# Optimization experiments

Hardware: AMD Instinct MI355X
Metric: run time of the kernel (lower is better)

Reference implementation:

```python
import jax, jax.numpy as jnp
import numpy as np

N, DIM, EMB = 8192, 128, 16
WIDTHS = [64, 32, 16]


def setup_inputs() -> dict:
    key = jax.random.key(0)
    ks = jax.random.split(key, 16)
    x = jax.random.normal(ks[0], (N, DIM), dtype=jnp.float32)
    dims = [DIM] + WIDTHS + [EMB]  # 128 -> 64 -> 32 -> 16 -> 16
    params = {}
    for i in range(4):
        fan_in, fan_out = dims[i], dims[i + 1]
        params[f"W{i+1}"] = jax.random.normal(ks[1 + 2 * i], (fan_in, fan_out), dtype=jnp.float32) * (1.0 / np.sqrt(fan_in))
        params[f"b{i+1}"] = jax.random.normal(ks[2 + 2 * i], (fan_out,), dtype=jnp.float32) * 0.01
    return {"x": x, **params}


def _encode(x, W1, b1, W2, b2, W3, b3, W4, b4):
    h = jax.nn.relu(x @ W1 + b1)
    h = jax.nn.relu(h @ W2 + b2)
    h = jax.nn.relu(h @ W3 + b3)
    return h @ W4 + b4  # [N, EMB]


def _tstudent_probs(z):
    # squared euclidean distances via the norm trick (avoids [N,N,EMB] tensor)
    sq = jnp.sum(z * z, axis=1)  # [N]
    dist = jnp.maximum(sq[:, None] + sq[None, :] - 2.0 * (z @ z.T), 0.0)  # [N,N]
    numerator = 1.0 / (1.0 + dist)
    return numerator / jnp.sum(numerator, axis=1, keepdims=True)


def reference(x, W1, b1, W2, b2, W3, b3, W4, b4):
    z = _encode(x, W1, b1, W2, b2, W3, b3, W4, b4)
    return _tstudent_probs(z)
```

## Files before the change

kernel.cpp:

```cpp
#include <hip/hip_runtime.h>

#define N 8192
#define DIM 128
#define NCHUNK 32

__global__ __launch_bounds__(64) void encoder_kernel(
    const float* __restrict__ x,
    const float* __restrict__ W1, const float* __restrict__ b1,
    const float* __restrict__ W2, const float* __restrict__ b2,
    const float* __restrict__ W3, const float* __restrict__ b3,
    const float* __restrict__ W4, const float* __restrict__ b4,
    float* __restrict__ z, float* __restrict__ sqout)
{
    __shared__ float sW2[64 * 32];
    __shared__ float sW3[32 * 16];
    __shared__ float sW4[16 * 16];
    __shared__ float sb1[64];
    __shared__ float sb2[32];
    __shared__ float sb3[16];
    __shared__ float sb4[16];
    __shared__ float sW1[128 * 64];
    __shared__ float sh1[64 * 65];

    int t = threadIdx.x;
    float* sh2 = sW1;
    float* sh3 = sW1 + 2112;

    for (int idx = t; idx < 128 * 64; idx += 64) sW1[idx] = W1[idx];
    for (int idx = t; idx < 64 * 32; idx += 64) sW2[idx] = W2[idx];
    for (int idx = t; idx < 32 * 16; idx += 64) sW3[idx] = W3[idx];
    for (int idx = t; idx < 16 * 16; idx += 64) sW4[idx] = W4[idx];
    sb1[t] = b1[t];
    if (t < 32) sb2[t] = b2[t];
    if (t < 16) { sb3[t] = b3[t]; sb4[t] = b4[t]; }
    __syncthreads();

    int row = blockIdx.x * 64 + t;
    const float4* xr = (const float4*)(x + (size_t)row * DIM);

    float h1[64];
    #pragma unroll
    for (int k = 0; k < 64; ++k) h1[k] = sb1[k];
    for (int j4 = 0; j4 < 32; ++j4) {
        float4 xv = xr[j4];
        const float* w0 = &sW1[(j4 * 4 + 0) * 64];
        const float* w1 = &sW1[(j4 * 4 + 1) * 64];
        const float* w2 = &sW1[(j4 * 4 + 2) * 64];
        const float* w3 = &sW1[(j4 * 4 + 3) * 64];
        #pragma unroll
        for (int k = 0; k < 64; ++k) h1[k] = fmaf(xv.x, w0[k], h1[k]);
        #pragma unroll
        for (int k = 0; k < 64; ++k) h1[k] = fmaf(xv.y, w1[k], h1[k]);
        #pragma unroll
        for (int k = 0; k < 64; ++k) h1[k] = fmaf(xv.z, w2[k], h1[k]);
        #pragma unroll
        for (int k = 0; k < 64; ++k) h1[k] = fmaf(xv.w, w3[k], h1[k]);
    }
    #pragma unroll
    for (int k = 0; k < 64; ++k) sh1[t * 65 + k] = fmaxf(h1[k], 0.0f);

    float h2[32];
    #pragma unroll
    for (int k = 0; k < 32; ++k) h2[k] = sb2[k];
    for (int j = 0; j < 64; ++j) {
        float a = sh1[t * 65 + j];
        #pragma unroll
        for (int k = 0; k < 32; ++k) h2[k] = fmaf(a, sW2[j * 32 + k], h2[k]);
    }
    #pragma unroll
    for (int k = 0; k < 32; ++k) sh2[t * 33 + k] = fmaxf(h2[k], 0.0f);

    float h3[16];
    #pragma unroll
    for (int k = 0; k < 16; ++k) h3[k] = sb3[k];
    for (int j = 0; j < 32; ++j) {
        float a = sh2[t * 33 + j];
        #pragma unroll
        for (int k = 0; k < 16; ++k) h3[k] = fmaf(a, sW3[j * 16 + k], h3[k]);
    }
    #pragma unroll
    for (int k = 0; k < 16; ++k) sh3[t * 17 + k] = fmaxf(h3[k], 0.0f);

    float zo[16];
    #pragma unroll
    for (int k = 0; k < 16; ++k) zo[k] = sb4[k];
    for (int j = 0; j < 16; ++j) {
        float a = sh3[t * 17 + j];
        #pragma unroll
        for (int k = 0; k < 16; ++k) zo[k] = fmaf(a, sW4[j * 16 + k], zo[k]);
    }

    float s = 0.0f;
    #pragma unroll
    for (int k = 0; k < 16; ++k) s = fmaf(zo[k], zo[k], s);
    sqout[row] = s;
    float4* zr = (float4*)(z + (size_t)row * 16);
    zr[0] = make_float4(zo[0], zo[1], zo[2], zo[3]);
    zr[1] = make_float4(zo[4], zo[5], zo[6], zo[7]);
    zr[2] = make_float4(zo[8], zo[9], zo[10], zo[11]);
    zr[3] = make_float4(zo[12], zo[13], zo[14], zo[15]);
}

__global__ __launch_bounds__(256) void pass1_kernel(
    const float* __restrict__ z, const float* __restrict__ sq,
    float* __restrict__ partial)
{
    __shared__ float s_zj[256 * 16];
    __shared__ float s_sqj[256];

    int t = threadIdx.x;
    int i0 = blockIdx.x * 256 + t;
    int i1 = i0 + 4096;
    int jb = blockIdx.y * 256;

    {
        const float4* src = (const float4*)(z + (size_t)(jb + t) * 16);
        float4* dst = (float4*)(s_zj + t * 16);
        dst[0] = src[0]; dst[1] = src[1]; dst[2] = src[2]; dst[3] = src[3];
        s_sqj[t] = sq[jb + t];
    }

    float zi0[16], zi1[16];
    {
        const float4* p0 = (const float4*)(z + (size_t)i0 * 16);
        const float4* p1 = (const float4*)(z + (size_t)i1 * 16);
        #pragma unroll
        for (int q = 0; q < 4; ++q) {
            float4 v0 = p0[q]; float4 v1 = p1[q];
            zi0[4*q] = v0.x; zi0[4*q+1] = v0.y; zi0[4*q+2] = v0.z; zi0[4*q+3] = v0.w;
            zi1[4*q] = v1.x; zi1[4*q+1] = v1.y; zi1[4*q+2] = v1.z; zi1[4*q+3] = v1.w;
        }
    }
    float sqi0 = sq[i0], sqi1 = sq[i1];
    __syncthreads();

    float acc0 = 0.0f, acc1 = 0.0f;
    #pragma unroll 4
    for (int jj = 0; jj < 256; ++jj) {
        const float* zj = s_zj + jj * 16;
        float d0 = 0.0f, d1 = 0.0f;
        #pragma unroll
        for (int k = 0; k < 16; ++k) {
            float w = zj[k];
            d0 = fmaf(zi0[k], w, d0);
            d1 = fmaf(zi1[k], w, d1);
        }
        float sj = s_sqj[jj];
        float dist0 = fmaxf(fmaf(-2.0f, d0, sqi0 + sj), 0.0f);
        float dist1 = fmaxf(fmaf(-2.0f, d1, sqi1 + sj), 0.0f);
        acc0 += __builtin_amdgcn_rcpf(1.0f + dist0);
        acc1 += __builtin_amdgcn_rcpf(1.0f + dist1);
    }
    partial[blockIdx.y * N + i0] = acc0;
    partial[blockIdx.y * N + i1] = acc1;
}

__global__ __launch_bounds__(256) void pass2_kernel(
    const float* __restrict__ z, const float* __restrict__ sq,
    const float* __restrict__ partial, float* __restrict__ out)
{
    __shared__ float s_zi[16 * 16];
    __shared__ float s_sqi[16];
    __shared__ float s_inv[16];
    __shared__ float s_red[16 * NCHUNK];

    int t = threadIdx.x;
    int ibase = blockIdx.x * 16;

    s_zi[t] = z[(size_t)ibase * 16 + t];
    if (t < 16) s_sqi[t] = sq[ibase + t];
    for (int q = t; q < 16 * NCHUNK; q += 256) {
        int ii = q >> 5;
        int c  = q & (NCHUNK - 1);
        s_red[ii * NCHUNK + c] = partial[(size_t)c * N + ibase + ii];
    }
    __syncthreads();
    if (t < 16) {
        float s = 0.0f;
        #pragma unroll
        for (int c = 0; c < NCHUNK; ++c) s += s_red[t * NCHUNK + c];
        s_inv[t] = 1.0f / s;
    }
    __syncthreads();

    for (int jb = 0; jb < N; jb += 256) {
        int j = jb + t;
        float zj[16];
        {
            const float4* zp = (const float4*)(z + (size_t)j * 16);
            #pragma unroll
            for (int q = 0; q < 4; ++q) {
                float4 v = zp[q];
                zj[4*q] = v.x; zj[4*q+1] = v.y; zj[4*q+2] = v.z; zj[4*q+3] = v.w;
            }
        }
        float sqj = sq[j];
        #pragma unroll
        for (int ii = 0; ii < 16; ++ii) {
            const float* zi = s_zi + ii * 16;
            float d = 0.0f;
            #pragma unroll
            for (int k = 0; k < 16; ++k) d = fmaf(zi[k], zj[k], d);
            float dist = fmaxf(fmaf(-2.0f, d, s_sqi[ii] + sqj), 0.0f);
            float num = __builtin_amdgcn_rcpf(1.0f + dist);
            __builtin_nontemporal_store(num * s_inv[ii],
                                        &out[(size_t)(ibase + ii) * N + j]);
        }
    }
}

extern "C" void kernel_launch(void* const* d_in, const int* in_sizes, int n_in,
                              void* d_out, int out_size, void* d_ws, size_t ws_size,
                              hipStream_t stream) {
    const float* x  = (const float*)d_in[0];
    const float* W1 = (const float*)d_in[1];
    const float* b1 = (const float*)d_in[2];
    const float* W2 = (const float*)d_in[3];
    const float* b2 = (const float*)d_in[4];
    const float* W3 = (const float*)d_in[5];
    const float* b3 = (const float*)d_in[6];
    const float* W4 = (const float*)d_in[7];
    const float* b4 = (const float*)d_in[8];
    float* out = (float*)d_out;

    float* ws = (float*)d_ws;
    float* z       = ws;
    float* sq      = ws + N * 16;
    float* partial = ws + N * 16 + N;

    encoder_kernel<<<128, 64, 0, stream>>>(x, W1, b1, W2, b2, W3, b3, W4, b4, z, sq);
    pass1_kernel<<<dim3(16, NCHUNK), 256, 0, stream>>>(z, sq, partial);
    pass2_kernel<<<N / 16, 256, 0, stream>>>(z, sq, partial, out);
}
```

Before: 395.6 us.

## Rework encoder split, pass1 register blocking, and pass2 vectorized stores

The encoder now splits each row's output columns across two half-waves and launches twice as many blocks, which cuts per-thread register arrays and raises parallelism. Pass1 processes four i-rows per thread over a smaller j tile with twice as many chunks, reusing each shared z_j load across more rows. Pass2 handles four rows per block, reduces the 64 partials with a wave shuffle, and has each thread produce four consecutive columns so it can issue 128-bit nontemporal stores. Pass2 now reads z_j directly from global memory per thread with a strided pattern, which may hurt coalescing, and the larger register footprint per thread may lower occupancy.

```diff
diff --git a/kernel.cpp b/kernel.cpp
--- a/kernel.cpp
+++ b/kernel.cpp
@@ -2,7 +2,10 @@
 
 #define N 8192
 #define DIM 128
-#define NCHUNK 32
+#define NCHUNK 64
+#define JTILE (N / NCHUNK)
+
+typedef float f32x4 __attribute__((ext_vector_type(4)));
 
 __global__ __launch_bounds__(64) void encoder_kernel(
     const float* __restrict__ x,
@@ -12,6 +15,7 @@
     const float* __restrict__ W4, const float* __restrict__ b4,
     float* __restrict__ z, float* __restrict__ sqout)
 {
+    __shared__ float sW1[128 * 64];
     __shared__ float sW2[64 * 32];
     __shared__ float sW3[32 * 16];
     __shared__ float sW4[16 * 16];
@@ -19,12 +23,13 @@
     __shared__ float sb2[32];
     __shared__ float sb3[16];
     __shared__ float sb4[16];
-    __shared__ float sW1[128 * 64];
-    __shared__ float sh1[64 * 65];
+    __shared__ float sh1[32 * 65];
+    __shared__ float sh2[32 * 33];
+    __shared__ float sh3[32 * 17];
 
     int t = threadIdx.x;
-    float* sh2 = sW1;
-    float* sh3 = sW1 + 2112;
+    int r = t & 31;
+    int h = t >> 5;
 
     for (int idx = t; idx < 128 * 64; idx += 64) sW1[idx] = W1[idx];
     for (int idx = t; idx < 64 * 32; idx += 64) sW2[idx] = W2[idx];
@@ -35,176 +40,199 @@
     if (t < 16) { sb3[t] = b3[t]; sb4[t] = b4[t]; }
     __syncthreads();
 
-    int row = blockIdx.x * 64 + t;
+    int row = blockIdx.x * 32 + r;
     const float4* xr = (const float4*)(x + (size_t)row * DIM);
 
-    float h1[64];
-    #pragma unroll
-    for (int k = 0; k < 64; ++k) h1[k] = sb1[k];
+    float h1[32];
+    #pragma unroll
+    for (int k = 0; k < 32; ++k) h1[k] = sb1[h * 32 + k];
     for (int j4 = 0; j4 < 32; ++j4) {
         float4 xv = xr[j4];
-        const float* w0 = &sW1[(j4 * 4 + 0) * 64];
-        const float* w1 = &sW1[(j4 * 4 + 1) * 64];
-        const float* w2 = &sW1[(j4 * 4 + 2) * 64];
-        const float* w3 = &sW1[(j4 * 4 + 3) * 64];
-        #pragma unroll
-        for (int k = 0; k < 64; ++k) h1[k] = fmaf(xv.x, w0[k], h1[k]);
-        #pragma unroll
-        for (int k = 0; k < 64; ++k) h1[k] = fmaf(xv.y, w1[k], h1[k]);
-        #pragma unroll
-        for (int k = 0; k < 64; ++k) h1[k] = fmaf(xv.z, w2[k], h1[k]);
-        #pragma unroll
-        for (int k = 0; k < 64; ++k) h1[k] = fmaf(xv.w, w3[k], h1[k]);
-    }
-    #pragma unroll
-    for (int k = 0; k < 64; ++k) sh1[t * 65 + k] = fmaxf(h1[k], 0.0f);
-
-    float h2[32];
-    #pragma unroll
-    for (int k = 0; k < 32; ++k) h2[k] = sb2[k];
+        const float* w0 = &sW1[(j4 * 4 + 0) * 64 + h * 32];
+        const float* w1 = &sW1[(j4 * 4 + 1) * 64 + h * 32];
+        const float* w2 = &sW1[(j4 * 4 + 2) * 64 + h * 32];
+        const float* w3 = &sW1[(j4 * 4 + 3) * 64 + h * 32];
+        #pragma unroll
+        for (int k = 0; k < 32; ++k) h1[k] = fmaf(xv.x, w0[k], h1[k]);
+        #pragma unroll
+        for (int k = 0; k < 32; ++k) h1[k] = fmaf(xv.y, w1[k], h1[k]);
+        #pragma unroll
+        for (int k = 0; k < 32; ++k) h1[k] = fmaf(xv.z, w2[k], h1[k]);
+        #pragma unroll
+        for (int k = 0; k < 32; ++k) h1[k] = fmaf(xv.w, w3[k], h1[k]);
+    }
+    #pragma unroll
+    for (int k = 0; k < 32; ++k) sh1[r * 65 + h * 32 + k] = fmaxf(h1[k], 0.0f);
+
+    float h2[16];
+    #pragma unroll
+    for (int k = 0; k < 16; ++k) h2[k] = sb2[h * 16 + k];
     for (int j = 0; j < 64; ++j) {
-        float a = sh1[t * 65 + j];
-        #pragma unroll
-        for (int k = 0; k < 32; ++k) h2[k] = fmaf(a, sW2[j * 32 + k], h2[k]);
-    }
-    #pragma unroll
-    for (int k = 0; k < 32; ++k) sh2[t * 33 + k] = fmaxf(h2[k], 0.0f);
-
-    float h3[16];
-    #pragma unroll
-    for (int k = 0; k < 16; ++k) h3[k] = sb3[k];
+        float a = sh1[r * 65 + j];
+        #pragma unroll
+        for (int k = 0; k < 16; ++k) h2[k] = fmaf(a, sW2[j * 32 + h * 16 + k], h2[k]);
+    }
+    #pragma unroll
+    for (int k = 0; k < 16; ++k) sh2[r * 33 + h * 16 + k] = fmaxf(h2[k], 0.0f);
+
+    float h3[8];
+    #pragma unroll
+    for (int k = 0; k < 8; ++k) h3[k] = sb3[h * 8 + k];
     for (int j = 0; j < 32; ++j) {
-        float a = sh2[t * 33 + j];
-        #pragma unroll
-        for (int k = 0; k < 16; ++k) h3[k] = fmaf(a, sW3[j * 16 + k], h3[k]);
-    }
-    #pragma unroll
-    for (int k = 0; k < 16; ++k) sh3[t * 17 + k] = fmaxf(h3[k], 0.0f);
-
-    float zo[16];
-    #pragma unroll
-    for (int k = 0; k < 16; ++k) zo[k] = sb4[k];
+        float a = sh2[r * 33 + j];
+        #pragma unroll
+        for (int k = 0; k < 8; ++k) h3[k] = fmaf(a, sW3[j * 16 + h * 8 + k], h3[k]);
+    }
+    #pragma unroll
+    for (int k = 0; k < 8; ++k) sh3[r * 17 + h * 8 + k] = fmaxf(h3[k], 0.0f);
+
+    float zo[8];
+    #pragma unroll
+    for (int k = 0; k < 8; ++k) zo[k] = sb4[h * 8 + k];
     for (int j = 0; j < 16; ++j) {
-        float a = sh3[t * 17 + j];
-        #pragma unroll
-        for (int k = 0; k < 16; ++k) zo[k] = fmaf(a, sW4[j * 16 + k], zo[k]);
+        float a = sh3[r * 17 + j];
+        #pragma unroll
+        for (int k = 0; k < 8; ++k) zo[k] = fmaf(a, sW4[j * 16 + h * 8 + k], zo[k]);
     }
 
     float s = 0.0f;
     #pragma unroll
-    for (int k = 0; k < 16; ++k) s = fmaf(zo[k], zo[k], s);
-    sqout[row] = s;
-    float4* zr = (float4*)(z + (size_t)row * 16);
+    for (int k = 0; k < 8; ++k) s = fmaf(zo[k], zo[k], s);
+    s += __shfl_xor(s, 32, 64);
+    if (h == 0) sqout[row] = s;
+    float4* zr = (float4*)(z + (size_t)row * 16 + h * 8);
     zr[0] = make_float4(zo[0], zo[1], zo[2], zo[3]);
     zr[1] = make_float4(zo[4], zo[5], zo[6], zo[7]);
-    zr[2] = make_float4(zo[8], zo[9], zo[10], zo[11]);
-    zr[3] = make_float4(zo[12], zo[13], zo[14], zo[15]);
 }
 
 __global__ __launch_bounds__(256) void pass1_kernel(
     const float* __restrict__ z, const float* __restrict__ sq,
     float* __restrict__ partial)
 {
-    __shared__ float s_zj[256 * 16];
-    __shared__ float s_sqj[256];
+    __shared__ float s_zj[JTILE * 16];
+    __shared__ float s_sqj[JTILE];
 
     int t = threadIdx.x;
     int i0 = blockIdx.x * 256 + t;
-    int i1 = i0 + 4096;
-    int jb = blockIdx.y * 256;
-
-    {
+    int jb = blockIdx.y * JTILE;
+
+    if (t < JTILE) {
         const float4* src = (const float4*)(z + (size_t)(jb + t) * 16);
         float4* dst = (float4*)(s_zj + t * 16);
         dst[0] = src[0]; dst[1] = src[1]; dst[2] = src[2]; dst[3] = src[3];
         s_sqj[t] = sq[jb + t];
     }
 
-    float zi0[16], zi1[16];
-    {
-        const float4* p0 = (const float4*)(z + (size_t)i0 * 16);
-        const float4* p1 = (const float4*)(z + (size_t)i1 * 16);
+    float zi[4][16];
+    float sqi[4];
+    #pragma unroll
+    for (int rr = 0; rr < 4; ++rr) {
+        const float4* p = (const float4*)(z + (size_t)(i0 + rr * 2048) * 16);
         #pragma unroll
         for (int q = 0; q < 4; ++q) {
-            float4 v0 = p0[q]; float4 v1 = p1[q];
-            zi0[4*q] = v0.x; zi0[4*q+1] = v0.y; zi0[4*q+2] = v0.z; zi0[4*q+3] = v0.w;
-            zi1[4*q] = v1.x; zi1[4*q+1] = v1.y; zi1[4*q+2] = v1.z; zi1[4*q+3] = v1.w;
-        }
-    }
-    float sqi0 = sq[i0], sqi1 = sq[i1];
+            float4 v = p[q];
+            zi[rr][4*q]   = v.x; zi[rr][4*q+1] = v.y;
+            zi[rr][4*q+2] = v.z; zi[rr][4*q+3] = v.w;
+        }
+        sqi[rr] = sq[i0 + rr * 2048];
+    }
     __syncthreads();
 
-    float acc0 = 0.0f, acc1 = 0.0f;
-    #pragma unroll 4
-    for (int jj = 0; jj < 256; ++jj) {
+    float acc0 = 0.0f, acc1 = 0.0f, acc2 = 0.0f, acc3 = 0.0f;
+    #pragma unroll 2
+    for (int jj = 0; jj < JTILE; ++jj) {
         const float* zj = s_zj + jj * 16;
-        float d0 = 0.0f, d1 = 0.0f;
+        float d0 = 0.0f, d1 = 0.0f, d2 = 0.0f, d3 = 0.0f;
         #pragma unroll
         for (int k = 0; k < 16; ++k) {
             float w = zj[k];
-            d0 = fmaf(zi0[k], w, d0);
-            d1 = fmaf(zi1[k], w, d1);
+            d0 = fmaf(zi[0][k], w, d0);
+            d1 = fmaf(zi[1][k], w, d1);
+            d2 = fmaf(zi[2][k], w, d2);
+            d3 = fmaf(zi[3][k], w, d3);
         }
         float sj = s_sqj[jj];
-        float dist0 = fmaxf(fmaf(-2.0f, d0, sqi0 + sj), 0.0f);
-        float dist1 = fmaxf(fmaf(-2.0f, d1, sqi1 + sj), 0.0f);
-        acc0 += __builtin_amdgcn_rcpf(1.0f + dist0);
-        acc1 += __builtin_amdgcn_rcpf(1.0f + dist1);
-    }
-    partial[blockIdx.y * N + i0] = acc0;
-    partial[blockIdx.y * N + i1] = acc1;
+        float t0 = fmaxf(fmaf(-2.0f, d0, sqi[0] + sj), 0.0f);
+        float t1 = fmaxf(fmaf(-2.0f, d1, sqi[1] + sj), 0.0f);
+        float t2 = fmaxf(fmaf(-2.0f, d2, sqi[2] + sj), 0.0f);
+        float t3 = fmaxf(fmaf(-2.0f, d3, sqi[3] + sj), 0.0f);
+        acc0 += __builtin_amdgcn_rcpf(1.0f + t0);
+        acc1 += __builtin_amdgcn_rcpf(1.0f + t1);
+        acc2 += __builtin_amdgcn_rcpf(1.0f + t2);
+        acc3 += __builtin_amdgcn_rcpf(1.0f + t3);
+    }
+    size_t pb = (size_t)blockIdx.y * N + i0;
+    partial[pb]            = acc0;
+    partial[pb + 1 * 2048] = acc1;
+    partial[pb + 2 * 2048] = acc2;
+    partial[pb + 3 * 2048] = acc3;
 }
 
 __global__ __launch_bounds__(256) void pass2_kernel(
     const float* __restrict__ z, const float* __restrict__ sq,
     const float* __restrict__ partial, float* __restrict__ out)
 {
-    __shared__ float s_zi[16 * 16];
-    __shared__ float s_sqi[16];
-    __shared__ float s_inv[16];
-    __shared__ float s_red[16 * NCHUNK];
+    __shared__ float s_inv[4];
 
     int t = threadIdx.x;
-    int ibase = blockIdx.x * 16;
-
-    s_zi[t] = z[(size_t)ibase * 16 + t];
-    if (t < 16) s_sqi[t] = sq[ibase + t];
-    for (int q = t; q < 16 * NCHUNK; q += 256) {
-        int ii = q >> 5;
-        int c  = q & (NCHUNK - 1);
-        s_red[ii * NCHUNK + c] = partial[(size_t)c * N + ibase + ii];
+    int ibase = blockIdx.x * 4;
+    int w = t >> 6, lane = t & 63;
+
+    {
+        float v = partial[(size_t)lane * N + ibase + w];
+        #pragma unroll
+        for (int off = 32; off > 0; off >>= 1) v += __shfl_xor(v, off, 64);
+        if (lane == 0) s_inv[w] = 1.0f / v;
+    }
+
+    float zi[4][16];
+    float sqi[4];
+    #pragma unroll
+    for (int rr = 0; rr < 4; ++rr) {
+        const float4* p = (const float4*)(z + (size_t)(ibase + rr) * 16);
+        #pragma unroll
+        for (int q = 0; q < 4; ++q) {
+            float4 v = p[q];
+            zi[rr][4*q]   = v.x; zi[rr][4*q+1] = v.y;
+            zi[rr][4*q+2] = v.z; zi[rr][4*q+3] = v.w;
+        }
+        sqi[rr] = sq[ibase + rr];
     }
     __syncthreads();
-    if (t < 16) {
-        float s = 0.0f;
-        #pragma unroll
-        for (int c = 0; c < NCHUNK; ++c) s += s_red[t * NCHUNK + c];
-        s_inv[t] = 1.0f / s;
-    }
-    __syncthreads();
-
-    for (int jb = 0; jb < N; jb += 256) {
-        int j = jb + t;
-        float zj[16];
-        {
-            const float4* zp = (const float4*)(z + (size_t)j * 16);
+    float inv[4];
+    #pragma unroll
+    for (int rr = 0; rr < 4; ++rr) inv[rr] = s_inv[rr];
+
+    for (int jb = 0; jb < N; jb += 1024) {
+        int j0 = jb + t * 4;
+        float zj[4][16];
+        #pragma unroll
+        for (int q = 0; q < 4; ++q) {
+            const float4* p = (const float4*)(z + (size_t)(j0 + q) * 16);
+            #pragma unroll
+            for (int qq = 0; qq < 4; ++qq) {
+                float4 v = p[qq];
+                zj[q][4*qq]   = v.x; zj[q][4*qq+1] = v.y;
+                zj[q][4*qq+2] = v.z; zj[q][4*qq+3] = v.w;
+            }
+        }
+        float4 sqjv = *(const float4*)(sq + j0);
+        float sqj[4] = {sqjv.x, sqjv.y, sqjv.z, sqjv.w};
+
+        #pragma unroll
+        for (int rr = 0; rr < 4; ++rr) {
+            float dd[4];
             #pragma unroll
             for (int q = 0; q < 4; ++q) {
-                float4 v = zp[q];
-                zj[4*q] = v.x; zj[4*q+1] = v.y; zj[4*q+2] = v.z; zj[4*q+3] = v.w;
+                float d = 0.0f;
+                #pragma unroll
+                for (int k = 0; k < 16; ++k) d = fmaf(zi[rr][k], zj[q][k], d);
+                float dist = fmaxf(fmaf(-2.0f, d, sqi[rr] + sqj[q]), 0.0f);
+                dd[q] = __builtin_amdgcn_rcpf(1.0f + dist) * inv[rr];
             }
-        }
-        float sqj = sq[j];
-        #pragma unroll
-        for (int ii = 0; ii < 16; ++ii) {
-            const float* zi = s_zi + ii * 16;
-            float d = 0.0f;
-            #pragma unroll
-            for (int k = 0; k < 16; ++k) d = fmaf(zi[k], zj[k], d);
-            float dist = fmaxf(fmaf(-2.0f, d, s_sqi[ii] + sqj), 0.0f);
-            float num = __builtin_amdgcn_rcpf(1.0f + dist);
-            __builtin_nontemporal_store(num * s_inv[ii],
-                                        &out[(size_t)(ibase + ii) * N + j]);
+            f32x4 rv = {dd[0], dd[1], dd[2], dd[3]};
+            __builtin_nontemporal_store(rv,
+                (f32x4*)(out + (size_t)(ibase + rr) * N + j0));
         }
     }
 }
@@ -225,10 +253,10 @@
 
     float* ws = (float*)d_ws;
     float* z       = ws;
-    float* sq      = ws + N * 16;
+    float* sqv     = ws + N * 16;
     float* partial = ws + N * 16 + N;
 
-    encoder_kernel<<<128, 64, 0, stream>>>(x, W1, b1, W2, b2, W3, b3, W4, b4, z, sq);
-    pass1_kernel<<<dim3(16, NCHUNK), 256, 0, stream>>>(z, sq, partial);
-    pass2_kernel<<<N / 16, 256, 0, stream>>>(z, sq, partial, out);
-}
+    encoder_kernel<<<256, 64, 0, stream>>>(x, W1, b1, W2, b2, W3, b3, W4, b4, z, sqv);
+    pass1_kernel<<<dim3(8, NCHUNK), 256, 0, stream>>>(z, sqv, partial);
+    pass2_kernel<<<N / 4, 256, 0, stream>>>(z, sqv, partial, out);
+}
```

Result: slower. 435.5 us (+10.1%).
